# Performance work log

Hardware: AMD Instinct MI355X
Metric: run time of the kernel (lower is better)

## Reference

```python
import jax, jax.numpy as jnp
import numpy as np

D_MODEL = 2048
D_HEAD = 128
N_HEADS = D_MODEL // D_HEAD
SEQ_LENS = (512, 768, 384, 384)  # packed varlen sequences, sum = 2048
L_TOTAL = sum(SEQ_LENS)
EPS = 1e-6


def setup_inputs() -> dict:
    key = jax.random.key(0)
    ks = jax.random.split(key, 8)
    x = jax.random.normal(ks[0], (L_TOTAL, D_MODEL), jnp.float32)
    # Flux-style rope table: pairwise-duplicated cos/sin, pe = concat([cos, sin], -1) -> (L, 2*d_head)
    half = D_HEAD // 2
    pos = np.arange(L_TOTAL, dtype=np.float32)[:, None]
    freqs = 1.0 / (10000.0 ** (np.arange(half, dtype=np.float32) / half))  # (half,)
    ang = pos * freqs[None, :]                      # (L, half)
    cos = np.repeat(np.cos(ang), 2, axis=-1)        # (L, d_head), duplicated per pair
    sin = np.repeat(np.sin(ang), 2, axis=-1)
    pe = jnp.asarray(np.concatenate([cos, sin], axis=-1))  # (L, 2*d_head)
    seq_lens = jnp.asarray(SEQ_LENS, dtype=jnp.int32)
    std = 0.02
    qkv_w = std * jax.random.truncated_normal(ks[1], -2.0, 2.0, (3 * D_MODEL, D_MODEL), jnp.float32)
    qkv_b = jnp.zeros((3 * D_MODEL,), jnp.float32)
    q_scale = jnp.ones((D_HEAD,), jnp.float32)
    k_scale = jnp.ones((D_HEAD,), jnp.float32)
    proj_w = std * jax.random.truncated_normal(ks[2], -2.0, 2.0, (D_MODEL, D_MODEL), jnp.float32)
    proj_b = jnp.zeros((D_MODEL,), jnp.float32)
    return {"x": x, "pe": pe, "seq_lens": seq_lens, "qkv_w": qkv_w, "qkv_b": qkv_b,
            "q_scale": q_scale, "k_scale": k_scale, "proj_w": proj_w, "proj_b": proj_b}


def _rms_norm(t, scale):
    tf = t.astype(jnp.float32)
    rrms = jax.lax.rsqrt(jnp.mean(tf * tf, axis=-1, keepdims=True) + EPS)
    return (tf * rrms * scale).astype(t.dtype)


def _apply_rope(t, pe):
    # t: (L, nh, dh); pe: (L, 2*dh) with pairwise-duplicated cos|sin
    L, nh, dh = t.shape
    c = pe[:, None, 0:dh:2]     # (L, 1, dh/2) per-pair cos
    s = pe[:, None, dh::2]      # (L, 1, dh/2) per-pair sin
    tr = t.reshape(L, nh, dh // 2, 2)
    t1, t2 = tr[..., 0], tr[..., 1]
    out = jnp.stack([t1 * c - t2 * s, t1 * s + t2 * c], axis=-1)
    return out.reshape(L, nh, dh)


def reference(x, pe, seq_lens, qkv_w, qkv_b, q_scale, k_scale, proj_w, proj_b):
    L = x.shape[0]
    qkv = x @ qkv_w.T + qkv_b                      # (L, 3*D)
    q, k, v = jnp.split(qkv, 3, axis=-1)
    q = q.reshape(L, N_HEADS, D_HEAD)
    k = k.reshape(L, N_HEADS, D_HEAD)
    v = v.reshape(L, N_HEADS, D_HEAD)
    q = _rms_norm(q, q_scale)
    k = _rms_norm(k, k_scale)
    q = _apply_rope(q, pe)
    k = _apply_rope(k, pe)
    # block-diagonal (packed varlen) attention
    n = seq_lens.shape[0]
    seg = jnp.repeat(jnp.arange(n, dtype=jnp.int32), seq_lens, total_repeat_length=L)  # (L,)
    mask = seg[:, None] == seg[None, :]            # (L, L) block-diagonal
    scale = 1.0 / jnp.sqrt(jnp.float32(D_HEAD))
    scores = jnp.einsum('lhd,mhd->hlm', q, k) * scale  # (nh, L, L)
    scores = jnp.where(mask[None], scores, jnp.finfo(scores.dtype).min)
    p = jax.nn.softmax(scores, axis=-1)
    out = jnp.einsum('hlm,mhd->lhd', p, v)         # (L, nh, dh)
    out = out.reshape(L, D_MODEL)
    return out @ proj_w.T + proj_b
```

## Files before the change

kernel.cpp:

```cpp
#include <hip/hip_runtime.h>

typedef unsigned short ushort_t;
typedef __attribute__((ext_vector_type(4))) float f4;
typedef __attribute__((ext_vector_type(8))) short s8v;
typedef __attribute__((ext_vector_type(8))) __bf16 bf8v;

#define AS1 __attribute__((address_space(1)))
#define AS3 __attribute__((address_space(3)))

__device__ __forceinline__ void async16(void* lds, const void* g) {
    __builtin_amdgcn_global_load_lds((AS1 const void*)g, (AS3 void*)lds, 16, 0, 0);
}

__device__ __forceinline__ f4 mfma16(s8v a, s8v b, f4 c) {
    return __builtin_amdgcn_mfma_f32_16x16x32_bf16(
        __builtin_bit_cast(bf8v, a), __builtin_bit_cast(bf8v, b), c, 0, 0, 0);
}

__device__ __forceinline__ ushort_t f2bf(float f) {
    unsigned int u = __float_as_uint(f);
    u += 0x7fffu + ((u >> 16) & 1u);
    return (ushort_t)(u >> 16);
}
__device__ __forceinline__ float bf2f(ushort_t u) {
    return __uint_as_float(((unsigned int)u) << 16);
}

#define L_TOT   2048
#define DMODEL  2048
#define DHEAD   128
#define NHEADS  16

__global__ __launch_bounds__(256) void cast_all(const float* __restrict__ x,
                                                const float* __restrict__ w1,
                                                const float* __restrict__ w2,
                                                ushort_t* __restrict__ xo,
                                                ushort_t* __restrict__ w1o,
                                                ushort_t* __restrict__ w2o) {
    for (int i = blockIdx.x * 256 + threadIdx.x; i < 5242880; i += 2048 * 256) {
        const float* src; ushort_t* dst; int off;
        if (i < 1048576)      { src = x;  dst = xo;  off = 0; }
        else if (i < 4194304) { src = w1; dst = w1o; off = 1048576; }
        else                  { src = w2; dst = w2o; off = 4194304; }
        int j = i - off;
        float4 v = ((const float4*)src)[j];
        ushort4 o;
        o.x = f2bf(v.x); o.y = f2bf(v.y); o.z = f2bf(v.z); o.w = f2bf(v.w);
        ((ushort4*)dst)[j] = o;
    }
}


template <int P>
__device__ __forceinline__ void cluster(f4 (&acc)[8][4], const s8v (&af)[2][2],
                                        const s8v (&bf)[4][2]) {
    __builtin_amdgcn_s_setprio(1);
#pragma unroll
    for (int mm = 0; mm < 2; mm++)
#pragma unroll
        for (int nn = 0; nn < 4; nn++) {
            acc[2 * P + mm][nn] = mfma16(af[mm][0], bf[nn][0], acc[2 * P + mm][nn]);
            acc[2 * P + mm][nn] = mfma16(af[mm][1], bf[nn][1], acc[2 * P + mm][nn]);
        }
    __builtin_amdgcn_s_setprio(0);
}

#define LDF(base, row, oo) (*(const s8v*)&(base)[(row) * 64 + (oo)])

#define STG(dst, gb, Tt, h)                                                              \
    async16(&(dst)[tid * 8 + (2 * (h)) * 4096],                                          \
            (gb) + (size_t)(Tt) * 64 + (size_t)(128 * (h)) * K);                         \
    async16(&(dst)[tid * 8 + (2 * (h) + 1) * 4096],                                      \
            (gb) + (size_t)(Tt) * 64 + (size_t)(128 * (h) + 64) * K);

#define OPENB()                                                                          \
    __builtin_amdgcn_s_barrier();                                                        \
    asm volatile("s_waitcnt lgkmcnt(0)" ::: "memory");                                   \
    __builtin_amdgcn_sched_barrier(0);

#define TILE(cur, T)                                                                     \
    {                                                                                    \
        const int Tn1 = ((T) + 1 < NT) ? (T) + 1 : NT - 1;                               \
        const int Tn2 = ((T) + 2 < NT) ? (T) + 2 : NT - 1;                               \
        const ushort_t* fA = stA[cur];                                                   \
        const ushort_t* fB = stB[cur];                                                   \
        s8v bfrag[4][2];                                                                 \
        s8v afrag[2][2];                                                                 \
                                                                  \
        bfrag[0][0] = LDF(fB, brow + 0,  o0); bfrag[0][1] = LDF(fB, brow + 0,  o1);      \
        bfrag[1][0] = LDF(fB, brow + 16, o0); bfrag[1][1] = LDF(fB, brow + 16, o1);      \
        bfrag[2][0] = LDF(fB, brow + 32, o0); bfrag[2][1] = LDF(fB, brow + 32, o1);      \
        bfrag[3][0] = LDF(fB, brow + 48, o0); bfrag[3][1] = LDF(fB, brow + 48, o1);      \
        afrag[0][0] = LDF(fA, arow + 0,  o0); afrag[0][1] = LDF(fA, arow + 0,  o1);      \
        afrag[1][0] = LDF(fA, arow + 16, o0); afrag[1][1] = LDF(fA, arow + 16, o1);      \
        STG(stA[(cur) ^ 1], gA, Tn1, 0)                                                  \
        OPENB()                                                                          \
        cluster<0>(acc, afrag, bfrag);                                                   \
        __builtin_amdgcn_s_barrier();                                                    \
                                                                  \
        afrag[0][0] = LDF(fA, arow + 32, o0); afrag[0][1] = LDF(fA, arow + 32, o1);      \
        afrag[1][0] = LDF(fA, arow + 48, o0); afrag[1][1] = LDF(fA, arow + 48, o1);      \
        STG(stA[(cur) ^ 1], gA, Tn1, 1)                                                  \
        OPENB()                                                                          \
        cluster<1>(acc, afrag, bfrag);                                                   \
        __builtin_amdgcn_s_barrier();                                                    \
                                                                  \
        afrag[0][0] = LDF(fA, arow + 64, o0); afrag[0][1] = LDF(fA, arow + 64, o1);      \
        afrag[1][0] = LDF(fA, arow + 80, o0); afrag[1][1] = LDF(fA, arow + 80, o1);      \
        STG(stB[cur], gB, Tn2, 0)                                                        \
        OPENB()                                                                          \
        cluster<2>(acc, afrag, bfrag);                                                   \
        __builtin_amdgcn_s_barrier();                                                    \
                                                                  \
        afrag[0][0] = LDF(fA, arow + 96,  o0); afrag[0][1] = LDF(fA, arow + 96,  o1);    \
        afrag[1][0] = LDF(fA, arow + 112, o0); afrag[1][1] = LDF(fA, arow + 112, o1);    \
        STG(stB[cur], gB, Tn2, 1)                                                        \
        asm volatile("s_waitcnt vmcnt(4)" ::: "memory");                                 \
        __builtin_amdgcn_sched_barrier(0);                                               \
        OPENB()                                                                          \
        cluster<3>(acc, afrag, bfrag);                                                   \
        __builtin_amdgcn_s_barrier();                                                    \
    }

__global__ __launch_bounds__(512, 2) void gemm_qkv256(const ushort_t* __restrict__ A,
                                                      const ushort_t* __restrict__ Bt,
                                                      const float* __restrict__ bias,
                                                      ushort_t* __restrict__ qk_out,
                                                      ushort_t* __restrict__ vt_out,
                                                      int K) {
    __shared__ alignas(16) ushort_t sA[2][16384];
    __shared__ alignas(16) ushort_t sB[2][16384];

    const int tid  = threadIdx.x;
    const int lane = tid & 63;
    const int wave = tid >> 6;
    const int wm = wave >> 2;
    const int wn = wave & 3;

    const int phys = blockIdx.y * 8 + blockIdx.x;
    const int lid  = (phys & 7) * 24 + (phys >> 3);
    const int bxs  = lid & 7;
    const int bys  = lid >> 3;

    const int bm = bxs * 256;
    const int bn = bys * 256;
    const bool is_v = bys >= 16;
    const int NT = K >> 6;

    const int q15 = lane & 15;
    const int g   = lane >> 4;
    const int l7  = lane & 7;
    const int o0  = ((g    ) ^ l7) * 8;
    const int o1  = ((g + 4) ^ l7) * 8;
    const int arow = wm * 128 + q15;
    const int brow = wn * 64 + q15;

    const int rs  = tid >> 3;
    const int csw = ((tid & 7) ^ (rs & 7)) * 8;
    const ushort_t* Abase = A  + (size_t)(bm + rs) * K + csw;
    const ushort_t* Bbase = Bt + (size_t)(bn + rs) * K + csw;

    ushort_t* stA[2]; ushort_t* stB[2];
    const ushort_t* gA; const ushort_t* gB;
    if (!is_v) { stA[0] = sA[0]; stA[1] = sA[1]; stB[0] = sB[0]; stB[1] = sB[1];
                 gA = Abase; gB = Bbase; }
    else       { stA[0] = sB[0]; stA[1] = sB[1]; stB[0] = sA[0]; stB[1] = sA[1];
                 gA = Bbase; gB = Abase; }

    f4 acc[8][4];
#pragma unroll
    for (int i = 0; i < 8; i++)
#pragma unroll
        for (int j = 0; j < 4; j++) acc[i][j] = (f4){0.f, 0.f, 0.f, 0.f};

    STG(stA[0], gA, 0, 0) STG(stA[0], gA, 0, 1)
    STG(stB[0], gB, 0, 0) STG(stB[0], gB, 0, 1)
    {
        const int T1 = NT > 1 ? 1 : 0;
        STG(stB[1], gB, T1, 0) STG(stB[1], gB, T1, 1)
    }
    asm volatile("s_waitcnt vmcnt(4)" ::: "memory");
    __builtin_amdgcn_sched_barrier(0);
    __builtin_amdgcn_s_barrier();

    for (int T = 0; T < NT; T += 2) {
        TILE(0, T)
        TILE(1, T + 1)
    }

    if (!is_v) {
#pragma unroll
        for (int n = 0; n < 4; n++) {
            int col = bn + wn * 64 + n * 16 + q15;
            float bv = bias[col];
#pragma unroll
            for (int m = 0; m < 8; m++) {
                int r0 = bm + wm * 128 + m * 16 + g * 4;
#pragma unroll
                for (int r = 0; r < 4; r++)
                    qk_out[(size_t)(r0 + r) * 4096 + col] = f2bf(acc[m][n][r] + bv);
            }
        }
    } else {
        const int cb   = (bys - 16) * 256 + wm * 128;
        const int tok0 = bm + wn * 64 + q15;
#pragma unroll
        for (int m = 0; m < 8; m++) {
#pragma unroll
            for (int r = 0; r < 4; r++) {
                int c = cb + m * 16 + g * 4 + r;
                float bv = bias[4096 + c];
#pragma unroll
                for (int n = 0; n < 4; n++)
                    vt_out[(size_t)c * L_TOT + tok0 + n * 16] = f2bf(acc[m][n][r] + bv);
            }
        }
    }
}

__global__ __launch_bounds__(256) void gemm_proj(const ushort_t* __restrict__ A,
                                                 const ushort_t* __restrict__ Bt,
                                                 float* __restrict__ Cf,
                                                 int K) {
    __shared__ alignas(16) ushort_t pA[128 * 64];
    __shared__ alignas(16) ushort_t pB[128 * 64];
    const int tid  = threadIdx.x;
    const int lane = tid & 63;
    const int wave = tid >> 6;
    const int wr = (wave >> 1) * 64;
    const int wc = (wave & 1) * 64;
    const int bm = blockIdx.x * 128;
    const int bn = blockIdx.y * 128;

    f4 acc[4][4];
#pragma unroll
    for (int i = 0; i < 4; i++)
#pragma unroll
        for (int j = 0; j < 4; j++) acc[i][j] = (f4){0.f, 0.f, 0.f, 0.f};

    const int rs  = tid >> 3;
    const int csw = ((tid & 7) ^ (rs & 7)) * 8;
    const ushort_t* Abase = A  + (size_t)(bm + rs) * K + csw;
    const ushort_t* Bbase = Bt + (size_t)(bn + rs) * K + csw;
    const int arow = wr + (lane & 15);
    const int brow = wc + (lane & 15);
    const int l7 = lane & 7;
    const int o0 = (((lane >> 4)    ) ^ l7) * 8;
    const int o1 = (((lane >> 4) + 4) ^ l7) * 8;
    const int kbeg = blockIdx.z * (K >> 1);
    const int kend = kbeg + (K >> 1);

    for (int k0 = kbeg; k0 < kend; k0 += 64) {
#pragma unroll
        for (int s = 0; s < 4; s++) {
            async16(&pA[tid * 8 + s * 2048], Abase + k0 + (size_t)(32 * s) * K);
            async16(&pB[tid * 8 + s * 2048], Bbase + k0 + (size_t)(32 * s) * K);
        }
        __syncthreads();

        s8v af[4], bfr[4];
#pragma unroll
        for (int i = 0; i < 4; i++) af[i]  = *(const s8v*)&pA[(arow + i * 16) * 64 + o0];
#pragma unroll
        for (int j = 0; j < 4; j++) bfr[j] = *(const s8v*)&pB[(brow + j * 16) * 64 + o0];
#pragma unroll
        for (int i = 0; i < 4; i++)
#pragma unroll
            for (int j = 0; j < 4; j++) acc[i][j] = mfma16(af[i], bfr[j], acc[i][j]);

#pragma unroll
        for (int i = 0; i < 4; i++) af[i]  = *(const s8v*)&pA[(arow + i * 16) * 64 + o1];
#pragma unroll
        for (int j = 0; j < 4; j++) bfr[j] = *(const s8v*)&pB[(brow + j * 16) * 64 + o1];
#pragma unroll
        for (int i = 0; i < 4; i++)
#pragma unroll
            for (int j = 0; j < 4; j++) acc[i][j] = mfma16(af[i], bfr[j], acc[i][j]);
        __syncthreads();
    }

    const int q = lane & 15;
    const int g = lane >> 4;
    const int crow0 = bm + wr + g * 4;
    const int ccol0 = bn + wc + q;
    float* Cp = Cf + (size_t)blockIdx.z * L_TOT * DMODEL;
#pragma unroll
    for (int j = 0; j < 4; j++) {
        int col = ccol0 + j * 16;
#pragma unroll
        for (int i = 0; i < 4; i++) {
#pragma unroll
            for (int r = 0; r < 4; r++)
                Cp[(size_t)(crow0 + i * 16 + r) * DMODEL + col] = acc[i][j][r];
        }
    }
}

__global__ __launch_bounds__(256) void reduce_bias(const float* __restrict__ part,
                                                   const float* __restrict__ bias,
                                                   float* __restrict__ out) {
    int i = blockIdx.x * 256 + threadIdx.x;
    f4 a = ((const f4*)part)[i];
    f4 b = ((const f4*)(part + (size_t)L_TOT * DMODEL))[i];
    f4 bv = ((const f4*)bias)[i & 511];
    ((f4*)out)[i] = a + b + bv;
}

__global__ __launch_bounds__(256) void norm_rope(const ushort_t* __restrict__ qk,
                                                 const float* __restrict__ pe,
                                                 const float* __restrict__ q_scale,
                                                 const float* __restrict__ k_scale,
                                                 ushort_t* __restrict__ qh,
                                                 ushort_t* __restrict__ kh) {
    int wid  = blockIdx.x * 4 + (threadIdx.x >> 6);
    int lane = threadIdx.x & 63;
    int l = wid >> 4;
    int h = wid & 15;

    const ushort_t* base = qk + (size_t)l * 4096 + h * DHEAD + 2 * lane;
    ushort2 qu = *(const ushort2*)base;
    ushort2 ku = *(const ushort2*)(base + 2048);
    float qvx = bf2f(qu.x), qvy = bf2f(qu.y);
    float kvx = bf2f(ku.x), kvy = bf2f(ku.y);

    float qss = qvx * qvx + qvy * qvy;
    float kss = kvx * kvx + kvy * kvy;
#pragma unroll
    for (int m = 32; m >= 1; m >>= 1) {
        qss += __shfl_xor(qss, m);
        kss += __shfl_xor(kss, m);
    }
    float qr = rsqrtf(qss * (1.0f / DHEAD) + 1e-6f);
    float kr = rsqrtf(kss * (1.0f / DHEAD) + 1e-6f);

    float c = pe[(size_t)l * 256 + 2 * lane];
    float s = pe[(size_t)l * 256 + 128 + 2 * lane];

    float q1 = qvx * qr * q_scale[2 * lane];
    float q2 = qvy * qr * q_scale[2 * lane + 1];
    float k1 = kvx * kr * k_scale[2 * lane];
    float k2 = kvy * kr * k_scale[2 * lane + 1];

    const float sc = 0.08838834764831845f;
    float qo0 = (q1 * c - q2 * s) * sc;
    float qo1 = (q1 * s + q2 * c) * sc;
    float ko0 = k1 * c - k2 * s;
    float ko1 = k1 * s + k2 * c;

    size_t o = ((size_t)h * L_TOT + l) * DHEAD + 2 * lane;
    ushort2 qp, kp;
    qp.x = f2bf(qo0); qp.y = f2bf(qo1);
    kp.x = f2bf(ko0); kp.y = f2bf(ko1);
    *(ushort2*)(qh + o) = qp;
    *(ushort2*)(kh + o) = kp;
}

__global__ __launch_bounds__(256) void attn_kernel(const ushort_t* __restrict__ qh,
                                                   const ushort_t* __restrict__ kh,
                                                   const ushort_t* __restrict__ vt,
                                                   ushort_t* __restrict__ attn_out) {
    __shared__ alignas(16) ushort_t sK[2][64 * 128];
    __shared__ alignas(16) ushort_t sV[2][128 * 64];
    __shared__ alignas(16) ushort_t sP[4][16 * 64];

    const int phys = blockIdx.y * 32 + blockIdx.x;
    const int lid  = (phys & 7) * 64 + (phys >> 3);
    const int qt = lid & 31;
    const int h  = lid >> 5;

    const int tid = threadIdx.x;
    const int lane = tid & 63;
    const int w = tid >> 6;
    const int qrow0 = qt * 64 + w * 16;

    int q0 = qt * 64;
    int seg_start, seg_end;
    if (q0 < 512)       { seg_start = 0;    seg_end = 512;  }
    else if (q0 < 1280) { seg_start = 512;  seg_end = 1280; }
    else if (q0 < 1664) { seg_start = 1280; seg_end = 1664; }
    else                { seg_start = 1664; seg_end = 2048; }

    const int g = lane >> 4;
    const int q = lane & 15;
    const int qa7 = q & 7;

    const ushort_t* ksrc[4];
    const ushort_t* vsrc[4];
#pragma unroll
    for (int i = 0; i < 4; i++) {
        int p = i * 256 + tid;
        ksrc[i] = kh + ((size_t)h * L_TOT + (p >> 4)) * DHEAD + ((p & 15) ^ ((p >> 4) & 7)) * 8;
        vsrc[i] = vt + ((size_t)h * DHEAD + (p >> 3)) * L_TOT + ((p & 7) ^ ((p >> 3) & 7)) * 8;
    }

    s8v qf[4];
    {
        const ushort_t* qbase = qh + ((size_t)h * L_TOT + qrow0 + q) * DHEAD;
#pragma unroll
        for (int kd = 0; kd < 4; kd++) qf[kd] = *(const s8v*)(qbase + kd * 32 + g * 8);
    }

    f4 o[8];
#pragma unroll
    for (int j = 0; j < 8; j++) o[j] = (f4){0.f, 0.f, 0.f, 0.f};
    float lsum[4] = {0.f, 0.f, 0.f, 0.f};

#pragma unroll
    for (int i = 0; i < 4; i++) {
        int p = i * 256 + tid;
        async16(&sK[0][p * 8], ksrc[i] + (size_t)seg_start * DHEAD);
        async16(&sV[0][p * 8], vsrc[i] + seg_start);
    }

    int cur = 0;
    for (int kt = seg_start; kt < seg_end; kt += 64) {
        if (kt + 64 < seg_end) {
#pragma unroll
            for (int i = 0; i < 4; i++) {
                int p = i * 256 + tid;
                async16(&sK[cur ^ 1][p * 8], ksrc[i] + (size_t)(kt + 64) * DHEAD);
                async16(&sV[cur ^ 1][p * 8], vsrc[i] + (kt + 64));
            }
            asm volatile("s_waitcnt vmcnt(8)" ::: "memory");
        } else {
            asm volatile("s_waitcnt vmcnt(0)" ::: "memory");
        }
        __builtin_amdgcn_sched_barrier(0);
        __syncthreads();

        const ushort_t* Kc = sK[cur];
        const ushort_t* Vc = sV[cur];

        f4 S[4];
        __builtin_amdgcn_s_setprio(1);
#pragma unroll
        for (int tj = 0; tj < 4; tj++) {
            f4 st = (f4){0.f, 0.f, 0.f, 0.f};
#pragma unroll
            for (int kd = 0; kd < 4; kd++) {
                s8v bfrag = *(const s8v*)&Kc[(tj * 16 + q) * 128 + (((kd * 4 + g) ^ qa7) * 8)];
                st = mfma16(qf[kd], bfrag, st);
            }
            S[tj] = st;
        }
        __builtin_amdgcn_s_setprio(0);

#pragma unroll
        for (int tj = 0; tj < 4; tj++)
#pragma unroll
            for (int r = 0; r < 4; r++) {
                float p = __expf(S[tj][r]);
                S[tj][r] = p;
                lsum[r] += p;
            }

#pragma unroll
        for (int tj = 0; tj < 4; tj++) {
            int cg = tj * 2 + (q >> 3);
#pragma unroll
            for (int r = 0; r < 4; r++) {
                int prow = g * 4 + r;
                sP[w][prow * 64 + ((cg ^ (prow & 7)) * 8) + qa7] = f2bf(S[tj][r]);
            }
        }
        asm volatile("s_waitcnt lgkmcnt(0)" ::: "memory");

        __builtin_amdgcn_s_setprio(1);
#pragma unroll
        for (int ks = 0; ks < 2; ks++) {
            s8v pf = *(const s8v*)&sP[w][q * 64 + (((ks * 4 + g) ^ qa7) * 8)];
#pragma unroll
            for (int j = 0; j < 8; j++) {
                s8v vf = *(const s8v*)&Vc[(j * 16 + q) * 64 + (((ks * 4 + g) ^ qa7) * 8)];
                o[j] = mfma16(pf, vf, o[j]);
            }
        }
        __builtin_amdgcn_s_setprio(0);
        __syncthreads();
        cur ^= 1;
    }

#pragma unroll
    for (int r = 0; r < 4; r++) {
        float rs = lsum[r];
        rs += __shfl_xor(rs, 1);
        rs += __shfl_xor(rs, 2);
        rs += __shfl_xor(rs, 4);
        rs += __shfl_xor(rs, 8);
        int row = qrow0 + g * 4 + r;
        float inv = 1.0f / rs;
#pragma unroll
        for (int j = 0; j < 8; j++) {
            attn_out[(size_t)row * DMODEL + h * DHEAD + j * 16 + q] = f2bf(o[j][r] * inv);
        }
    }
}

extern "C" void kernel_launch(void* const* d_in, const int* in_sizes, int n_in,
                              void* d_out, int out_size, void* d_ws, size_t ws_size,
                              hipStream_t stream) {
    const float* x       = (const float*)d_in[0];
    const float* pe      = (const float*)d_in[1];
    const float* qkv_w   = (const float*)d_in[3];
    const float* qkv_b   = (const float*)d_in[4];
    const float* q_scale = (const float*)d_in[5];
    const float* k_scale = (const float*)d_in[6];
    const float* proj_w  = (const float*)d_in[7];
    const float* proj_b  = (const float*)d_in[8];
    float* out = (float*)d_out;

    char* ws = (char*)d_ws;
    const size_t MB = 1024 * 1024;
    ushort_t* x_bf     = (ushort_t*)(ws + 0);
    ushort_t* wqkv_bf  = (ushort_t*)(ws + 8 * MB);
    ushort_t* wproj_bf = (ushort_t*)(ws + 32 * MB);
    ushort_t* qk_bf    = (ushort_t*)(ws + 40 * MB);
    ushort_t* qh       = (ushort_t*)(ws + 57 * MB);
    ushort_t* kh       = (ushort_t*)(ws + 65 * MB);
    ushort_t* vt       = (ushort_t*)(ws + 73 * MB);
    ushort_t* attn_b   = (ushort_t*)(ws + 81 * MB);
    float*    part     = (float*)   (ws + 40 * MB);

    cast_all<<<2048, 256, 0, stream>>>(x, qkv_w, proj_w, x_bf, wqkv_bf, wproj_bf);

    gemm_qkv256<<<dim3(8, 24), 512, 0, stream>>>(x_bf, wqkv_bf, qkv_b, qk_bf, vt, 2048);

    norm_rope<<<8192, 256, 0, stream>>>(qk_bf, pe, q_scale, k_scale, qh, kh);

    attn_kernel<<<dim3(32, 16), 256, 0, stream>>>(qh, kh, vt, attn_b);

    gemm_proj<<<dim3(16, 16, 2), 256, 0, stream>>>(attn_b, wproj_bf, part, 2048);
    reduce_bias<<<4096, 256, 0, stream>>>(part, proj_b, out);
}
```

Baseline: 255.1 us.

## Fuse RMS-norm and RoPE into QKV GEMM epilogue; overlap proj weight cast

Removes the separate norm_rope kernel. The QKV GEMM epilogue now adds the bias, does the per-head RMS reduction using shuffles plus an LDS exchange between wave pairs, applies RoPE with a lane-pair shuffle, and writes head-major Q/K directly. The proj weight cast moves out of cast_all into 64 extra blocks of the QKV GEMM grid so it runs alongside the GEMM tiles. The GEMM launch-bounds occupancy hint is also dropped. This saves a bf16 qk round trip and one launch, at the cost of scattered 2-byte epilogue stores, per-element pe loads, and possible register pressure.

```diff
diff --git a/kernel.cpp b/kernel.cpp
--- a/kernel.cpp
+++ b/kernel.cpp
@@ -33,15 +33,12 @@
 
 __global__ __launch_bounds__(256) void cast_all(const float* __restrict__ x,
                                                 const float* __restrict__ w1,
-                                                const float* __restrict__ w2,
                                                 ushort_t* __restrict__ xo,
-                                                ushort_t* __restrict__ w1o,
-                                                ushort_t* __restrict__ w2o) {
-    for (int i = blockIdx.x * 256 + threadIdx.x; i < 5242880; i += 2048 * 256) {
+                                                ushort_t* __restrict__ w1o) {
+    for (int i = blockIdx.x * 256 + threadIdx.x; i < 4194304; i += 2048 * 256) {
         const float* src; ushort_t* dst; int off;
         if (i < 1048576)      { src = x;  dst = xo;  off = 0; }
-        else if (i < 4194304) { src = w1; dst = w1o; off = 1048576; }
-        else                  { src = w2; dst = w2o; off = 4194304; }
+        else                  { src = w1; dst = w1o; off = 1048576; }
         int j = i - off;
         float4 v = ((const float4*)src)[j];
         ushort4 o;
@@ -122,12 +119,18 @@
         __builtin_amdgcn_s_barrier();                                                    \
     }
 
-__global__ __launch_bounds__(512, 2) void gemm_qkv256(const ushort_t* __restrict__ A,
-                                                      const ushort_t* __restrict__ Bt,
-                                                      const float* __restrict__ bias,
-                                                      ushort_t* __restrict__ qk_out,
-                                                      ushort_t* __restrict__ vt_out,
-                                                      int K) {
+__global__ __launch_bounds__(512) void gemm_qkv256(const ushort_t* __restrict__ A,
+                                                   const ushort_t* __restrict__ Bt,
+                                                   const float* __restrict__ bias,
+                                                   const float* __restrict__ pe,
+                                                   const float* __restrict__ q_scale,
+                                                   const float* __restrict__ k_scale,
+                                                   const float* __restrict__ projw,
+                                                   ushort_t* __restrict__ projw_bf,
+                                                   ushort_t* __restrict__ qh,
+                                                   ushort_t* __restrict__ kh,
+                                                   ushort_t* __restrict__ vt_out,
+                                                   int K) {
     __shared__ alignas(16) ushort_t sA[2][16384];
     __shared__ alignas(16) ushort_t sB[2][16384];
 
@@ -138,9 +141,26 @@
     const int wn = wave & 3;
 
     const int phys = blockIdx.y * 8 + blockIdx.x;
-    const int lid  = (phys & 7) * 24 + (phys >> 3);
-    const int bxs  = lid & 7;
-    const int bys  = lid >> 3;
+    const int lid  = (phys & 7) * 32 + (phys >> 3);
+    const int xcd  = lid >> 5;
+    const int slot = lid & 31;
+
+    if (slot >= 24) {
+        const int ci = xcd * 8 + (slot - 24);
+#pragma unroll
+        for (int it = 0; it < 32; it++) {
+            int j = ci * 16384 + it * 512 + tid;
+            float4 v = ((const float4*)projw)[j];
+            ushort4 o;
+            o.x = f2bf(v.x); o.y = f2bf(v.y); o.z = f2bf(v.z); o.w = f2bf(v.w);
+            ((ushort4*)projw_bf)[j] = o;
+        }
+        return;
+    }
+
+    const int gid = xcd * 24 + slot;
+    const int bxs = gid & 7;
+    const int bys = gid >> 3;
 
     const int bm = bxs * 256;
     const int bn = bys * 256;
@@ -188,17 +208,68 @@
         TILE(1, T + 1)
     }
 
+    asm volatile("s_waitcnt vmcnt(0)" ::: "memory");
+    __syncthreads();
+
     if (!is_v) {
+        const int col0 = bn + wn * 64;
 #pragma unroll
         for (int n = 0; n < 4; n++) {
-            int col = bn + wn * 64 + n * 16 + q15;
-            float bv = bias[col];
+            float bv = bias[col0 + n * 16 + q15];
+#pragma unroll
+            for (int m = 0; m < 8; m++)
+#pragma unroll
+                for (int r = 0; r < 4; r++) acc[m][n][r] += bv;
+        }
+        float sown[8][4];
+        float* red = (float*)sA;
+#pragma unroll
+        for (int m = 0; m < 8; m++) {
+            f4 sv;
+#pragma unroll
+            for (int r = 0; r < 4; r++) {
+                float s = 0.f;
+#pragma unroll
+                for (int n = 0; n < 4; n++) s += acc[m][n][r] * acc[m][n][r];
+                s += __shfl_xor(s, 1); s += __shfl_xor(s, 2);
+                s += __shfl_xor(s, 4); s += __shfl_xor(s, 8);
+                sown[m][r] = s; sv[r] = s;
+            }
+            if (q15 == m) *(f4*)&red[wave * 128 + m * 16 + g * 4] = sv;
+        }
+        __syncthreads();
+        float rrms[8][4];
+#pragma unroll
+        for (int m = 0; m < 8; m++) {
+            f4 pv = *(const f4*)&red[(wave ^ 1) * 128 + m * 16 + g * 4];
+#pragma unroll
+            for (int r = 0; r < 4; r++)
+                rrms[m][r] = rsqrtf((sown[m][r] + pv[r]) * (1.0f / 128.0f) + 1e-6f);
+        }
+        const bool isQ = bn < 2048;
+        ushort_t* dst = isQ ? qh : kh;
+        const float* scl = isQ ? q_scale : k_scale;
+        const float scq = isQ ? 0.08838834764831845f : 1.0f;
+        const int hbase = col0 - (isQ ? 0 : 2048);
+        const int odd = q15 & 1;
+#pragma unroll
+        for (int n = 0; n < 4; n++) {
+            const int head = (hbase + n * 16) >> 7;
+            const int dd   = ((hbase + n * 16) & 127) + q15;
+            const int i2   = dd & ~1;
+            const float scd = scl[dd] * scq;
 #pragma unroll
             for (int m = 0; m < 8; m++) {
-                int r0 = bm + wm * 128 + m * 16 + g * 4;
-#pragma unroll
-                for (int r = 0; r < 4; r++)
-                    qk_out[(size_t)(r0 + r) * 4096 + col] = f2bf(acc[m][n][r] + bv);
+#pragma unroll
+                for (int r = 0; r < 4; r++) {
+                    const int l = bm + wm * 128 + m * 16 + g * 4 + r;
+                    float c = pe[(size_t)l * 256 + i2];
+                    float s = pe[(size_t)l * 256 + 128 + i2];
+                    float v = acc[m][n][r] * rrms[m][r] * scd;
+                    float vp = __shfl_xor(v, 1);
+                    float out = odd ? (v * c + vp * s) : (v * c - vp * s);
+                    dst[((size_t)head * L_TOT + l) * DHEAD + dd] = f2bf(out);
+                }
             }
         }
     } else {
@@ -306,55 +377,6 @@
     ((f4*)out)[i] = a + b + bv;
 }
 
-__global__ __launch_bounds__(256) void norm_rope(const ushort_t* __restrict__ qk,
-                                                 const float* __restrict__ pe,
-                                                 const float* __restrict__ q_scale,
-                                                 const float* __restrict__ k_scale,
-                                                 ushort_t* __restrict__ qh,
-                                                 ushort_t* __restrict__ kh) {
-    int wid  = blockIdx.x * 4 + (threadIdx.x >> 6);
-    int lane = threadIdx.x & 63;
-    int l = wid >> 4;
-    int h = wid & 15;
-
-    const ushort_t* base = qk + (size_t)l * 4096 + h * DHEAD + 2 * lane;
-    ushort2 qu = *(const ushort2*)base;
-    ushort2 ku = *(const ushort2*)(base + 2048);
-    float qvx = bf2f(qu.x), qvy = bf2f(qu.y);
-    float kvx = bf2f(ku.x), kvy = bf2f(ku.y);
-
-    float qss = qvx * qvx + qvy * qvy;
-    float kss = kvx * kvx + kvy * kvy;
-#pragma unroll
-    for (int m = 32; m >= 1; m >>= 1) {
-        qss += __shfl_xor(qss, m);
-        kss += __shfl_xor(kss, m);
-    }
-    float qr = rsqrtf(qss * (1.0f / DHEAD) + 1e-6f);
-    float kr = rsqrtf(kss * (1.0f / DHEAD) + 1e-6f);
-
-    float c = pe[(size_t)l * 256 + 2 * lane];
-    float s = pe[(size_t)l * 256 + 128 + 2 * lane];
-
-    float q1 = qvx * qr * q_scale[2 * lane];
-    float q2 = qvy * qr * q_scale[2 * lane + 1];
-    float k1 = kvx * kr * k_scale[2 * lane];
-    float k2 = kvy * kr * k_scale[2 * lane + 1];
-
-    const float sc = 0.08838834764831845f;
-    float qo0 = (q1 * c - q2 * s) * sc;
-    float qo1 = (q1 * s + q2 * c) * sc;
-    float ko0 = k1 * c - k2 * s;
-    float ko1 = k1 * s + k2 * c;
-
-    size_t o = ((size_t)h * L_TOT + l) * DHEAD + 2 * lane;
-    ushort2 qp, kp;
-    qp.x = f2bf(qo0); qp.y = f2bf(qo1);
-    kp.x = f2bf(ko0); kp.y = f2bf(ko1);
-    *(ushort2*)(qh + o) = qp;
-    *(ushort2*)(kh + o) = kp;
-}
-
 __global__ __launch_bounds__(256) void attn_kernel(const ushort_t* __restrict__ qh,
                                                    const ushort_t* __restrict__ kh,
                                                    const ushort_t* __restrict__ vt,
@@ -514,18 +536,17 @@
     ushort_t* x_bf     = (ushort_t*)(ws + 0);
     ushort_t* wqkv_bf  = (ushort_t*)(ws + 8 * MB);
     ushort_t* wproj_bf = (ushort_t*)(ws + 32 * MB);
-    ushort_t* qk_bf    = (ushort_t*)(ws + 40 * MB);
     ushort_t* qh       = (ushort_t*)(ws + 57 * MB);
     ushort_t* kh       = (ushort_t*)(ws + 65 * MB);
     ushort_t* vt       = (ushort_t*)(ws + 73 * MB);
     ushort_t* attn_b   = (ushort_t*)(ws + 81 * MB);
     float*    part     = (float*)   (ws + 40 * MB);
 
-    cast_all<<<2048, 256, 0, stream>>>(x, qkv_w, proj_w, x_bf, wqkv_bf, wproj_bf);
-
-    gemm_qkv256<<<dim3(8, 24), 512, 0, stream>>>(x_bf, wqkv_bf, qkv_b, qk_bf, vt, 2048);
-
-    norm_rope<<<8192, 256, 0, stream>>>(qk_bf, pe, q_scale, k_scale, qh, kh);
+    cast_all<<<2048, 256, 0, stream>>>(x, qkv_w, x_bf, wqkv_bf);
+
+    gemm_qkv256<<<dim3(8, 32), 512, 0, stream>>>(x_bf, wqkv_bf, qkv_b, pe,
+                                                 q_scale, k_scale, proj_w, wproj_bf,
+                                                 qh, kh, vt, 2048);
 
     attn_kernel<<<dim3(32, 16), 256, 0, stream>>>(qh, kh, vt, attn_b);
 
```

After: 322.3 us. 1.26x slower.

## Move proj weight cast into extra blocks of the QKV GEMM launch

Applied to the files above, without the earlier changes.

The proj_w fp32-to-bf16 conversion is removed from the standalone cast kernel and done by 64 extra blocks appended to the QKV GEMM grid (8 per XCD slot group). The GEMM has only 192 tiles on a 256-CU part, so idle CUs can do the cast alongside the GEMM instead of serially beforehand. The block-to-tile remap is rewritten so each XCD gets 24 GEMM tiles plus 8 cast blocks. The extra blocks may compete with GEMM tiles for bandwidth or CU slots.

```diff
diff --git a/kernel.cpp b/kernel.cpp
--- a/kernel.cpp
+++ b/kernel.cpp
@@ -33,15 +33,12 @@
 
 __global__ __launch_bounds__(256) void cast_all(const float* __restrict__ x,
                                                 const float* __restrict__ w1,
-                                                const float* __restrict__ w2,
                                                 ushort_t* __restrict__ xo,
-                                                ushort_t* __restrict__ w1o,
-                                                ushort_t* __restrict__ w2o) {
-    for (int i = blockIdx.x * 256 + threadIdx.x; i < 5242880; i += 2048 * 256) {
+                                                ushort_t* __restrict__ w1o) {
+    for (int i = blockIdx.x * 256 + threadIdx.x; i < 4194304; i += 2048 * 256) {
         const float* src; ushort_t* dst; int off;
         if (i < 1048576)      { src = x;  dst = xo;  off = 0; }
-        else if (i < 4194304) { src = w1; dst = w1o; off = 1048576; }
-        else                  { src = w2; dst = w2o; off = 4194304; }
+        else                  { src = w1; dst = w1o; off = 1048576; }
         int j = i - off;
         float4 v = ((const float4*)src)[j];
         ushort4 o;
@@ -125,6 +122,8 @@
 __global__ __launch_bounds__(512, 2) void gemm_qkv256(const ushort_t* __restrict__ A,
                                                       const ushort_t* __restrict__ Bt,
                                                       const float* __restrict__ bias,
+                                                      const float* __restrict__ projw,
+                                                      ushort_t* __restrict__ projw_bf,
                                                       ushort_t* __restrict__ qk_out,
                                                       ushort_t* __restrict__ vt_out,
                                                       int K) {
@@ -138,9 +137,26 @@
     const int wn = wave & 3;
 
     const int phys = blockIdx.y * 8 + blockIdx.x;
-    const int lid  = (phys & 7) * 24 + (phys >> 3);
-    const int bxs  = lid & 7;
-    const int bys  = lid >> 3;
+    const int lid  = (phys & 7) * 32 + (phys >> 3);
+    const int xcd  = lid >> 5;
+    const int slot = lid & 31;
+
+    if (slot >= 24) {
+        const int ci = xcd * 8 + (slot - 24);
+#pragma unroll
+        for (int it = 0; it < 32; it++) {
+            int j = ci * 16384 + it * 512 + tid;
+            float4 v = ((const float4*)projw)[j];
+            ushort4 o;
+            o.x = f2bf(v.x); o.y = f2bf(v.y); o.z = f2bf(v.z); o.w = f2bf(v.w);
+            ((ushort4*)projw_bf)[j] = o;
+        }
+        return;
+    }
+
+    const int gid = xcd * 24 + slot;
+    const int bxs = gid & 7;
+    const int bys = gid >> 3;
 
     const int bm = bxs * 256;
     const int bn = bys * 256;
@@ -521,9 +537,11 @@
     ushort_t* attn_b   = (ushort_t*)(ws + 81 * MB);
     float*    part     = (float*)   (ws + 40 * MB);
 
-    cast_all<<<2048, 256, 0, stream>>>(x, qkv_w, proj_w, x_bf, wqkv_bf, wproj_bf);
-
-    gemm_qkv256<<<dim3(8, 24), 512, 0, stream>>>(x_bf, wqkv_bf, qkv_b, qk_bf, vt, 2048);
+    cast_all<<<2048, 256, 0, stream>>>(x, qkv_w, x_bf, wqkv_bf);
+
+    gemm_qkv256<<<dim3(8, 32), 512, 0, stream>>>(x_bf, wqkv_bf, qkv_b,
+                                                 proj_w, wproj_bf,
+                                                 qk_bf, vt, 2048);
 
     norm_rope<<<8192, 256, 0, stream>>>(qk_bf, pe, q_scale, k_scale, qh, kh);
 
```

Result: faster. 248.9 us (-2.4%).
